# Optimization experiments

Hardware: AMD Instinct MI355X
Metric: run time of the kernel (lower is better)

The kernel has to match this reference:

```python
import jax, jax.numpy as jnp
import numpy as np

D, C, H, W = 8, 512, 64, 64


def setup_inputs() -> dict:
    key = jax.random.key(0)
    k1, k2, k3 = jax.random.split(key, 3)
    x = jax.random.normal(k1, (D, C, H, W), dtype=jnp.float32)
    atten = jax.random.normal(k2, (D, C, C), dtype=jnp.float32)
    gamma = jax.random.normal(k3, (1,), dtype=jnp.float32)
    return {"x": x, "atten": atten, "gamma": gamma}


def reference(x, atten, gamma):
    d, c, h, w = x.shape
    q = x.reshape(d, c, h * w)              # q == v == flattened x; k = q^T
    # energy[d, i, j] = <channel_i, channel_j> over spatial positions
    energy = jnp.einsum('din,djn->dij', q, q)
    # max-centering: rowmax - energy (note the sign flip vs standard softmax)
    energy_new = jnp.max(energy, axis=-1, keepdims=True) - energy
    attention = jax.nn.softmax(energy_new, axis=-1)
    attention = jax.nn.softmax(attention + atten, axis=-1)
    # out = attention^T @ v : out[d, j, n] = sum_i attention[d, i, j] * v[d, i, n]
    out = jnp.einsum('dij,din->djn', attention, q).reshape(d, c, h, w)
    return gamma * out + x
```

## Files before the change

### kernel.cpp

```cpp
#include <hip/hip_runtime.h>
#include <hip/hip_bf16.h>

#define DD 8
#define CC 512
#define NN 4096

typedef __bf16 bf16x8 __attribute__((ext_vector_type(8)));
typedef float  f32x4  __attribute__((ext_vector_type(4)));
typedef ushort ush8   __attribute__((ext_vector_type(8)));

__device__ __forceinline__ ushort f2bf(float f) {
  unsigned u = __float_as_uint(f);
  u = (u + 0x7fffu + ((u >> 16) & 1u)) >> 16;
  return (ushort)u;
}
__device__ __forceinline__ float bf2f(ushort h) {
  return __uint_as_float(((unsigned)h) << 16);
}

__device__ __forceinline__ void gl_lds16(const ushort* g, ushort* l) {
  __builtin_amdgcn_global_load_lds(
      (const __attribute__((address_space(1))) void*)g,
      (__attribute__((address_space(3))) void*)l, 16, 0, 0);
}

__global__ __launch_bounds__(256) void k0_convert(
    const float* __restrict__ x, ushort* __restrict__ qh,
    ushort* __restrict__ ql, ushort* __restrict__ qt) {
  int d = blockIdx.z, ct = blockIdx.y, nt = blockIdx.x;
  __shared__ ushort T[64][68];
  int t = threadIdx.x;
  int rr = t >> 4;
  int c4 = (t & 15) * 4;
  const float* xb = x + ((size_t)(d * CC + ct * 64)) * NN + nt * 64;
#pragma unroll
  for (int it = 0; it < 4; ++it) {
    int r = it * 16 + rr;
    float4 v = *(const float4*)(xb + (size_t)r * NN + c4);
    ushort h0 = f2bf(v.x), h1 = f2bf(v.y), h2 = f2bf(v.z), h3 = f2bf(v.w);
    ushort l0 = f2bf(v.x - bf2f(h0)), l1 = f2bf(v.y - bf2f(h1));
    ushort l2 = f2bf(v.z - bf2f(h2)), l3 = f2bf(v.w - bf2f(h3));
    size_t qi = ((size_t)(d * CC + ct * 64 + r)) * NN + nt * 64 + c4;
    *(ushort4*)(qh + qi) = make_ushort4(h0, h1, h2, h3);
    *(ushort4*)(ql + qi) = make_ushort4(l0, l1, l2, l3);
    *(ushort4*)&T[r][c4] = make_ushort4(h0, h1, h2, h3);
  }
  __syncthreads();
#pragma unroll
  for (int it = 0; it < 4; ++it) {
    int nl = it * 16 + rr;
    ushort4 v = make_ushort4(T[c4 + 0][nl], T[c4 + 1][nl], T[c4 + 2][nl], T[c4 + 3][nl]);
    *(ushort4*)(qt + ((size_t)(d * NN + nt * 64 + nl)) * CC + ct * 64 + c4) = v;
  }
}

__global__ __launch_bounds__(256, 2) void k1_gram(
    const ushort* __restrict__ qh, const ushort* __restrict__ ql,
    float* __restrict__ Ep, int ns, int nkk, int ksp) {
  __shared__ ushort As[2][128 * 32];
  __shared__ ushort Bs[2][128 * 32];
  int b = blockIdx.x;
  int s = b % ns;
  int rem = b / ns;
  int tile = rem % 10, d = rem / 10;
  int tm = (int)((0x3221110000ULL >> (tile * 4)) & 15ULL);
  int tn = (int)((0x3323213210ULL >> (tile * 4)) & 15ULL);
  int t = threadIdx.x, lane = t & 63, w = t >> 6;
  int wm = (w >> 1) * 64, wn = (w & 1) * 64;
  int qd = lane >> 4, fr = lane & 15;

  const ushort* srcbase = (w & 1) ? ql : qh;
  int rowblk = (w < 2) ? tm : tn;
  const ushort* gsrc = srcbase +
      ((size_t)(d * CC + rowblk * 128 + (lane >> 2))) * NN +
      (size_t)s * ksp + (lane & 3) * 8;
  ushort* ldst = (w < 2) ? As[w & 1] : Bs[w & 1];

  f32x4 acc[4][4];
#pragma unroll
  for (int i = 0; i < 4; ++i)
#pragma unroll
    for (int j = 0; j < 4; ++j) acc[i][j] = (f32x4){0.f, 0.f, 0.f, 0.f};

  for (int kk = 0; kk < nkk; ++kk) {
    __syncthreads();
    const ushort* g0 = gsrc + (size_t)kk * 32;
#pragma unroll
    for (int c = 0; c < 8; ++c)
      gl_lds16(g0 + (size_t)c * 16 * NN, ldst + c * 512);
    __syncthreads();

    bf16x8 ah[4], al[4];
#pragma unroll
    for (int mi = 0; mi < 4; ++mi) {
      int off = (wm + mi * 16 + fr) * 32 + qd * 8;
      ah[mi] = *(const bf16x8*)&As[0][off];
      al[mi] = *(const bf16x8*)&As[1][off];
    }
#pragma unroll
    for (int ni = 0; ni < 4; ++ni) {
      int off = (wn + ni * 16 + fr) * 32 + qd * 8;
      bf16x8 bh = *(const bf16x8*)&Bs[0][off];
      bf16x8 bl = *(const bf16x8*)&Bs[1][off];
#pragma unroll
      for (int mi = 0; mi < 4; ++mi) {
        acc[mi][ni] = __builtin_amdgcn_mfma_f32_16x16x32_bf16(ah[mi], bh, acc[mi][ni], 0, 0, 0);
        acc[mi][ni] = __builtin_amdgcn_mfma_f32_16x16x32_bf16(ah[mi], bl, acc[mi][ni], 0, 0, 0);
        acc[mi][ni] = __builtin_amdgcn_mfma_f32_16x16x32_bf16(al[mi], bh, acc[mi][ni], 0, 0, 0);
      }
    }
  }

  size_t ebase = ((size_t)(s * DD + d)) * ((size_t)CC * CC);
#pragma unroll
  for (int mi = 0; mi < 4; ++mi) {
    int r0 = tm * 128 + wm + mi * 16 + qd * 4;
#pragma unroll
    for (int ni = 0; ni < 4; ++ni) {
      int c0 = tn * 128 + wn + ni * 16 + fr;
      float* ep = Ep + ebase + (size_t)r0 * CC + c0;
#pragma unroll
      for (int r = 0; r < 4; ++r) ep[(size_t)r * CC] = acc[mi][ni][r];
    }
  }
  if (tm != tn) {
#pragma unroll
    for (int mi = 0; mi < 4; ++mi) {
      int r0 = tm * 128 + wm + mi * 16 + qd * 4;
#pragma unroll
      for (int ni = 0; ni < 4; ++ni) {
        int c0 = tn * 128 + wn + ni * 16 + fr;
        float4 v = make_float4(acc[mi][ni][0], acc[mi][ni][1],
                               acc[mi][ni][2], acc[mi][ni][3]);
        *(float4*)(Ep + ebase + (size_t)c0 * CC + r0) = v;
      }
    }
  }
}

__device__ __forceinline__ float wmin(float v) {
#pragma unroll
  for (int o = 32; o > 0; o >>= 1) v = fminf(v, __shfl_xor(v, o));
  return v;
}
__device__ __forceinline__ float wmax(float v) {
#pragma unroll
  for (int o = 32; o > 0; o >>= 1) v = fmaxf(v, __shfl_xor(v, o));
  return v;
}
__device__ __forceinline__ float wsum(float v) {
#pragma unroll
  for (int o = 32; o > 0; o >>= 1) v += __shfl_xor(v, o);
  return v;
}

__global__ __launch_bounds__(256) void k2_softmax(
    const float* __restrict__ Ep, const float* __restrict__ atten,
    ushort* __restrict__ a2t, int ns) {
  int d = blockIdx.y, i0 = blockIdx.x * 8;
  int t = threadIdx.x, lane = t & 63, w = t >> 6;
  int j8 = lane * 8;
  __shared__ ushort T[8][520];
  const size_t SP = (size_t)DD * CC * CC;

#pragma unroll
  for (int r2 = 0; r2 < 2; ++r2) {
    int ri = w * 2 + r2;
    size_t base = ((size_t)(d * CC + i0 + ri)) * CC + j8;
    f32x4 a0 = (f32x4){0.f, 0.f, 0.f, 0.f};
    f32x4 a1 = (f32x4){0.f, 0.f, 0.f, 0.f};
    for (int s = 0; s < ns; ++s) {
      const float* p = Ep + (size_t)s * SP + base;
      a0 += *(const f32x4*)p;
      a1 += *(const f32x4*)(p + 4);
    }
    float mn = fminf(fminf(fminf(a0[0], a0[1]), fminf(a0[2], a0[3])),
                     fminf(fminf(a1[0], a1[1]), fminf(a1[2], a1[3])));
    mn = wmin(mn);
    float p0 = __expf(mn - a0[0]), p1 = __expf(mn - a0[1]);
    float p2 = __expf(mn - a0[2]), p3 = __expf(mn - a0[3]);
    float p4 = __expf(mn - a1[0]), p5 = __expf(mn - a1[1]);
    float p6 = __expf(mn - a1[2]), p7 = __expf(mn - a1[3]);
    float s1 = wsum(p0 + p1 + p2 + p3 + p4 + p5 + p6 + p7);
    float inv1 = 1.0f / s1;
    const float* ap = atten + base;
    f32x4 t0 = *(const f32x4*)ap;
    f32x4 t1 = *(const f32x4*)(ap + 4);
    float u0 = p0 * inv1 + t0[0], u1 = p1 * inv1 + t0[1];
    float u2 = p2 * inv1 + t0[2], u3 = p3 * inv1 + t0[3];
    float u4 = p4 * inv1 + t1[0], u5 = p5 * inv1 + t1[1];
    float u6 = p6 * inv1 + t1[2], u7 = p7 * inv1 + t1[3];
    float mx = wmax(fmaxf(fmaxf(fmaxf(u0, u1), fmaxf(u2, u3)),
                          fmaxf(fmaxf(u4, u5), fmaxf(u6, u7))));
    float q0 = __expf(u0 - mx), q1 = __expf(u1 - mx);
    float q2 = __expf(u2 - mx), q3 = __expf(u3 - mx);
    float q4 = __expf(u4 - mx), q5 = __expf(u5 - mx);
    float q6 = __expf(u6 - mx), q7 = __expf(u7 - mx);
    float s2 = wsum(q0 + q1 + q2 + q3 + q4 + q5 + q6 + q7);
    float inv2 = 1.0f / s2;
    ush8 o;
    o[0] = f2bf(q0 * inv2); o[1] = f2bf(q1 * inv2);
    o[2] = f2bf(q2 * inv2); o[3] = f2bf(q3 * inv2);
    o[4] = f2bf(q4 * inv2); o[5] = f2bf(q5 * inv2);
    o[6] = f2bf(q6 * inv2); o[7] = f2bf(q7 * inv2);
    *(ush8*)&T[ri][j8] = o;
  }
  __syncthreads();
#pragma unroll
  for (int it = 0; it < 2; ++it) {
    int j = t + it * 256;
    ush8 o;
#pragma unroll
    for (int k = 0; k < 8; ++k) o[k] = T[k][j];
    *(ush8*)&a2t[((size_t)(d * CC + j)) * CC + i0] = o;
  }
}

__global__ __launch_bounds__(256, 2) void k3_out(
    const ushort* __restrict__ a2t, const ushort* __restrict__ qt,
    const float* __restrict__ x, const float* __restrict__ gamma,
    float* __restrict__ out) {
  __shared__ ushort As[128 * 32];
  __shared__ ushort Bs[128 * 32];
  int b = blockIdx.x;
  int nt = b & 31, jt = (b >> 5) & 3, d = b >> 7;
  int t = threadIdx.x, lane = t & 63, w = t >> 6;
  int wj = (w >> 1) * 64, wn2 = (w & 1) * 64;
  int qd = lane >> 4, fr = lane & 15;

  const ushort* src = (w < 2)
      ? (a2t + (size_t)d * CC * CC + (size_t)(jt * 128) * CC)
      : (qt + (size_t)d * NN * CC + (size_t)(nt * 128) * CC);
  ushort* ldst = (w < 2) ? As : Bs;
  int cbase = (w & 1) * 4;
  const ushort* g0 = src + ((size_t)(cbase * 16 + (lane >> 2))) * CC + (lane & 3) * 8;
  ushort* l0 = ldst + cbase * 16 * 32;

  f32x4 acc[4][4];
#pragma unroll
  for (int i = 0; i < 4; ++i)
#pragma unroll
    for (int j = 0; j < 4; ++j) acc[i][j] = (f32x4){0.f, 0.f, 0.f, 0.f};

  for (int kk = 0; kk < CC / 32; ++kk) {
    __syncthreads();
#pragma unroll
    for (int c = 0; c < 4; ++c)
      gl_lds16(g0 + kk * 32 + (size_t)(c * 16) * CC, l0 + c * 512);
    __syncthreads();

    bf16x8 qf[4];
#pragma unroll
    for (int ii = 0; ii < 4; ++ii)
      qf[ii] = *(const bf16x8*)&Bs[(wn2 + ii * 16 + fr) * 32 + qd * 8];
#pragma unroll
    for (int jj = 0; jj < 4; ++jj) {
      bf16x8 af = *(const bf16x8*)&As[(wj + jj * 16 + fr) * 32 + qd * 8];
#pragma unroll
      for (int ii = 0; ii < 4; ++ii)
        acc[ii][jj] = __builtin_amdgcn_mfma_f32_16x16x32_bf16(qf[ii], af, acc[ii][jj], 0, 0, 0);
    }
  }

  float g = gamma[0];
#pragma unroll
  for (int ii = 0; ii < 4; ++ii) {
    int n0 = nt * 128 + wn2 + ii * 16 + qd * 4;
#pragma unroll
    for (int jj = 0; jj < 4; ++jj) {
      int j = jt * 128 + wj + jj * 16 + fr;
      size_t idx = ((size_t)(d * CC + j)) * NN + n0;
      float4 xv = *(const float4*)(x + idx);
      float4 ov = make_float4(g * acc[ii][jj][0] + xv.x,
                              g * acc[ii][jj][1] + xv.y,
                              g * acc[ii][jj][2] + xv.z,
                              g * acc[ii][jj][3] + xv.w);
      *(float4*)(out + idx) = ov;
    }
  }
}

extern "C" void kernel_launch(void* const* d_in, const int* in_sizes, int n_in,
                              void* d_out, int out_size, void* d_ws, size_t ws_size,
                              hipStream_t stream) {
  (void)in_sizes; (void)n_in; (void)out_size;
  const float* x     = (const float*)d_in[0];
  const float* atten = (const float*)d_in[1];
  const float* gamma = (const float*)d_in[2];
  float* out = (float*)d_out;

  char* ws = (char*)d_ws;
  ushort* qh  = (ushort*)(ws);
  ushort* ql  = (ushort*)(ws + 33554432);
  ushort* qt  = (ushort*)(ws + 67108864);
  ushort* a2t = (ushort*)(ws + 100663296);
  float*  Ep  = (float*) (ws + 104857600);

  int ns = (ws_size >= 104857600ULL + 8ULL * 8388608ULL) ? 8 : 4;
  int ksp = NN / ns;
  int nkk = ksp / 32;

  k0_convert<<<dim3(64, 8, 8), 256, 0, stream>>>(x, qh, ql, qt);
  k1_gram   <<<dim3(80 * ns), 256, 0, stream>>>(qh, ql, Ep, ns, nkk, ksp);
  k2_softmax<<<dim3(64, 8), 256, 0, stream>>>(Ep, atten, a2t, ns);
  k3_out    <<<dim3(1024), 256, 0, stream>>>(a2t, qt, x, gamma, out);
}
```

Measured before the change: 235.0 us.

## Widen convert kernel with XOR-swizzled LDS transpose, reorder gram blocks, raise occupancy

The conversion kernel now handles 8 elements per thread and writes 16-byte bf16 vectors. Its LDS transpose tile drops padding in favour of an XOR chunk swizzle, which cuts store instructions and aims to avoid bank conflicts. The gram kernel's block index decomposition is reordered so consecutive blocks cover different tiles of the same K-split, which changes L2 locality. The gram and output GEMM kernels get a launch_bounds minimum of 4 blocks per SM instead of 2, which may force register spilling.

```diff
diff --git a/kernel.cpp b/kernel.cpp
--- a/kernel.cpp
+++ b/kernel.cpp
@@ -28,41 +28,56 @@
     const float* __restrict__ x, ushort* __restrict__ qh,
     ushort* __restrict__ ql, ushort* __restrict__ qt) {
   int d = blockIdx.z, ct = blockIdx.y, nt = blockIdx.x;
-  __shared__ ushort T[64][68];
+  __shared__ ushort T[64][64];
   int t = threadIdx.x;
-  int rr = t >> 4;
-  int c4 = (t & 15) * 4;
+  int rr = t >> 3;
+  int j  = t & 7;
+  int n8 = j * 8;
   const float* xb = x + ((size_t)(d * CC + ct * 64)) * NN + nt * 64;
 #pragma unroll
-  for (int it = 0; it < 4; ++it) {
-    int r = it * 16 + rr;
-    float4 v = *(const float4*)(xb + (size_t)r * NN + c4);
-    ushort h0 = f2bf(v.x), h1 = f2bf(v.y), h2 = f2bf(v.z), h3 = f2bf(v.w);
-    ushort l0 = f2bf(v.x - bf2f(h0)), l1 = f2bf(v.y - bf2f(h1));
-    ushort l2 = f2bf(v.z - bf2f(h2)), l3 = f2bf(v.w - bf2f(h3));
-    size_t qi = ((size_t)(d * CC + ct * 64 + r)) * NN + nt * 64 + c4;
-    *(ushort4*)(qh + qi) = make_ushort4(h0, h1, h2, h3);
-    *(ushort4*)(ql + qi) = make_ushort4(l0, l1, l2, l3);
-    *(ushort4*)&T[r][c4] = make_ushort4(h0, h1, h2, h3);
+  for (int it = 0; it < 2; ++it) {
+    int r = it * 32 + rr;
+    const float* xr = xb + (size_t)r * NN + n8;
+    float4 v0 = *(const float4*)xr;
+    float4 v1 = *(const float4*)(xr + 4);
+    float vv[8] = {v0.x, v0.y, v0.z, v0.w, v1.x, v1.y, v1.z, v1.w};
+    ush8 h, l;
+#pragma unroll
+    for (int k = 0; k < 8; ++k) {
+      ushort hh = f2bf(vv[k]);
+      h[k] = hh;
+      l[k] = f2bf(vv[k] - bf2f(hh));
+    }
+    size_t qi = ((size_t)(d * CC + ct * 64 + r)) * NN + nt * 64 + n8;
+    *(ush8*)(qh + qi) = h;
+    *(ush8*)(ql + qi) = l;
+    *(ush8*)&T[r][(j ^ (r >> 3)) * 8] = h;
   }
   __syncthreads();
 #pragma unroll
-  for (int it = 0; it < 4; ++it) {
-    int nl = it * 16 + rr;
-    ushort4 v = make_ushort4(T[c4 + 0][nl], T[c4 + 1][nl], T[c4 + 2][nl], T[c4 + 3][nl]);
-    *(ushort4*)(qt + ((size_t)(d * NN + nt * 64 + nl)) * CC + ct * 64 + c4) = v;
-  }
-}
-
-__global__ __launch_bounds__(256, 2) void k1_gram(
+  for (int it = 0; it < 2; ++it) {
+    int n = it * 32 + rr;
+    int c8 = n8;
+    ush8 o;
+#pragma unroll
+    for (int cc = 0; cc < 8; ++cc) {
+      int c = c8 + cc;
+      int chunk = (n >> 3) ^ (c >> 3);
+      o[cc] = T[c][chunk * 8 + (n & 7)];
+    }
+    *(ush8*)&qt[((size_t)(d * NN + nt * 64 + n)) * CC + ct * 64 + c8] = o;
+  }
+}
+
+__global__ __launch_bounds__(256, 4) void k1_gram(
     const ushort* __restrict__ qh, const ushort* __restrict__ ql,
     float* __restrict__ Ep, int ns, int nkk, int ksp) {
   __shared__ ushort As[2][128 * 32];
   __shared__ ushort Bs[2][128 * 32];
   int b = blockIdx.x;
-  int s = b % ns;
-  int rem = b / ns;
-  int tile = rem % 10, d = rem / 10;
+  int tile = b % 10;
+  int rem = b / 10;
+  int s = rem % ns, d = rem / ns;
   int tm = (int)((0x3221110000ULL >> (tile * 4)) & 15ULL);
   int tn = (int)((0x3323213210ULL >> (tile * 4)) & 15ULL);
   int t = threadIdx.x, lane = t & 63, w = t >> 6;
@@ -216,7 +231,7 @@
   }
 }
 
-__global__ __launch_bounds__(256, 2) void k3_out(
+__global__ __launch_bounds__(256, 4) void k3_out(
     const ushort* __restrict__ a2t, const ushort* __restrict__ qt,
     const float* __restrict__ x, const float* __restrict__ gamma,
     float* __restrict__ out) {
```

Measured after the change: 279.6 us. +19.0%, slower.
